# Optimization experiments

Hardware: AMD Instinct MI355X
Metric: run time of the kernel (lower is better)

Reference implementation:

```python
import jax, jax.numpy as jnp
import numpy as np

N = 100_000      # nodes
E = 3_200_000    # edges
F_IN = 9
F_HID = 9
F_OUT = 1
EPS = 1e-5

def _ln(x, g, b):
    m = x.mean(-1, keepdims=True)
    v = x.var(-1, keepdims=True)
    return (x - m) / jnp.sqrt(v + EPS) * g + b

def _gat(x, src, dst, edge_attr, W, a_src, a_dst, We, a_e, bias):
    # Single-head GATConv with edge_dim=1, add_self_loops=True, fill_value='mean'
    n = x.shape[0]
    loop = jnp.arange(n)
    deg = jax.ops.segment_sum(jnp.ones((src.shape[0],), x.dtype), dst, n)
    loop_attr = jax.ops.segment_sum(edge_attr, dst, n) / jnp.maximum(deg, 1.0)[:, None]
    s = jnp.concatenate([src, loop])
    d = jnp.concatenate([dst, loop])
    ea = jnp.concatenate([edge_attr, loop_attr], axis=0)   # [E+N, 1]
    xp = x @ W                                             # [N, C]
    a = (xp * a_src).sum(-1)[s] + (xp * a_dst).sum(-1)[d] + ((ea @ We) * a_e).sum(-1)
    a = jax.nn.leaky_relu(a, 0.2)
    amax = jax.ops.segment_max(a, d, n)
    aexp = jnp.exp(a - amax[d])
    denom = jax.ops.segment_sum(aexp, d, n)
    alpha = aexp / (denom[d] + 1e-16)
    return jax.ops.segment_sum(alpha[:, None] * xp[s], d, n) + bias

def setup_inputs() -> dict:
    key = jax.random.key(0)
    ks = jax.random.split(key, 16)
    def rn(k, shp, s):
        return jax.random.normal(k, shp, jnp.float32) * s
    return {
        "x": jax.random.normal(ks[0], (N, F_IN), jnp.float32),
        "edge_index": jax.random.randint(ks[1], (2, E), 0, N, jnp.int32),
        "edge_attr": jax.random.normal(ks[2], (E, 1), jnp.float32),
        "ln1_g": jnp.ones((F_IN,), jnp.float32), "ln1_b": jnp.zeros((F_IN,), jnp.float32),
        "W0": rn(ks[3], (F_IN, F_HID), 0.3), "as0": rn(ks[4], (F_HID,), 0.3),
        "ad0": rn(ks[5], (F_HID,), 0.3), "We0": rn(ks[6], (1, F_HID), 0.3),
        "ae0": rn(ks[7], (F_HID,), 0.3), "b0": jnp.zeros((F_HID,), jnp.float32),
        "W1": rn(ks[8], (F_HID, F_HID), 0.3), "as1": rn(ks[9], (F_HID,), 0.3),
        "ad1": rn(ks[10], (F_HID,), 0.3), "We1": rn(ks[11], (1, F_HID), 0.3),
        "ae1": rn(ks[12], (F_HID,), 0.3), "b1": jnp.zeros((F_HID,), jnp.float32),
        "ng1": jnp.ones((F_HID,), jnp.float32), "nb1": jnp.zeros((F_HID,), jnp.float32),
        "ln2_g": jnp.ones((2 * F_HID,), jnp.float32), "ln2_b": jnp.zeros((2 * F_HID,), jnp.float32),
        "et_W": rn(ks[13], (2 * F_HID, F_HID), 0.2), "et_b": jnp.zeros((F_HID,), jnp.float32),
        "fc_W": rn(ks[14], (F_HID, F_OUT), 0.3), "fc_b": jnp.zeros((F_OUT,), jnp.float32),
        "att_W": rn(ks[15], (2 * F_OUT, F_OUT), 0.5), "att_b": jnp.zeros((F_OUT,), jnp.float32),
    }

def reference(x, edge_index, edge_attr, ln1_g, ln1_b, W0, as0, ad0, We0, ae0, b0,
              W1, as1, ad1, We1, ae1, b1, ng1, nb1, ln2_g, ln2_b,
              et_W, et_b, fc_W, fc_b, att_W, att_b):
    src, dst = edge_index[0], edge_index[1]
    h = _ln(x, ln1_g, ln1_b)
    # layer 0: no norm/residual
    h = jax.nn.leaky_relu(_gat(h, src, dst, edge_attr, W0, as0, ad0, We0, ae0, b0), 0.01)
    # layer 1: norm + residual
    ident = h
    h = _ln(_gat(h, src, dst, edge_attr, W1, as1, ad1, We1, ae1, b1), ng1, nb1) + ident
    h = jax.nn.leaky_relu(h, 0.01)
    # edge path: gather-concat-norm-MLP  [E, 2H]
    ef = _ln(jnp.concatenate([h[src], h[dst]], axis=1), ln2_g, ln2_b)
    eo = jax.nn.leaky_relu(ef @ et_W + et_b, 0.01)
    eo = eo @ fc_W + fc_b                       # [E, 1]
    # AttentionLayer
    comb = jnp.concatenate([eo, edge_attr], axis=1)   # [E, 2]
    w = jax.nn.softmax(comb @ att_W + att_b, axis=-1) # [E, 1]
    att = (w * comb).sum(axis=1, keepdims=True)       # [E, 1]
    return att + eo
```

## Files before the change

kernel.cpp:

```cpp
#include <hip/hip_runtime.h>
#include <hip/hip_bf16.h>
#include <hip/hip_fp16.h>

typedef __hip_bfloat16 bf16;
typedef unsigned int uint;
typedef unsigned short ushort;
#define TPB 256
#define TPBS 1024
#define TPBG 1024
#define BSH 7
#define BNODES 128
#define NBK_MAX 1024
#define CH 8192
#define EPT (CH / TPBS)
#define NW (TPBS / 64)
#define GPAD 16
#define CAP 4608

enum {
  LN1G = 0, LN1B = 9, PW0 = 18, AS0 = 99, AD0 = 108, CE0 = 117, B0 = 118,
  PW1 = 127, AS1 = 208, AD1 = 217, CE1 = 226, B1 = 227, NG = 236, NB = 245,
  LN2G = 254, LN2B = 272, ETW = 290, ETB = 452, FCW = 461, FCB = 470,
  GC = 471, KC = 480, NPARAM = 489
};

static __device__ __forceinline__ float lrelu(float x, float s) { return x >= 0.f ? x : s * x; }
static __device__ __forceinline__ float ldx(const void* p, long i, int isb) {
    return isb ? __bfloat162float(((const bf16*)p)[i]) : ((const float*)p)[i];
}
static __device__ __forceinline__ uint bfb(float f) {
    uint u = __float_as_uint(f);
    return (u + 0x7FFFu + ((u >> 16) & 1u)) >> 16;
}
static __device__ __forceinline__ uint pack2(float a, float b) { return bfb(a) | (bfb(b) << 16); }
static __device__ __forceinline__ float unlo(uint u) { return __uint_as_float(u << 16); }
static __device__ __forceinline__ float unhi(uint u) { return __uint_as_float(u & 0xFFFF0000u); }
static __device__ __forceinline__ ushort h16(float f) { return __half_as_ushort(__float2half(f)); }
static __device__ __forceinline__ uint p2h(float a, float b) { return (uint)h16(a) | ((uint)h16(b) << 16); }
static __device__ __forceinline__ float hfl(uint u) { return __half2float(__ushort_as_half((ushort)(u & 0xFFFFu))); }
static __device__ __forceinline__ float hfh(uint u) { return __half2float(__ushort_as_half((ushort)(u >> 16))); }
static __device__ __forceinline__ float hfs(ushort u) { return __half2float(__ushort_as_half(u)); }

__global__ void k_params(const void* ln1g, const void* ln1b,
                         const void* W0, const void* as0, const void* ad0,
                         const void* We0, const void* ae0, const void* b0,
                         const void* W1, const void* as1, const void* ad1,
                         const void* We1, const void* ae1, const void* b1,
                         const void* ng, const void* nb,
                         const void* ln2g, const void* ln2b,
                         const void* etW, const void* etb,
                         const void* fcW, const void* fcb,
                         float* __restrict__ P, int* __restrict__ flagp,
                         int* __restrict__ gcursor, int nbk)
{
    __shared__ int sflag;
    if (threadIdx.x == 0) {
        unsigned short h0 = ((const unsigned short*)ln1g)[0];
        sflag = (h0 == 0x3F80u) ? 1 : 0;
        *flagp = sflag;
    }
    __syncthreads();
    const int f = sflag;
    const int t = threadIdx.x;
    for (int j = t; j < nbk; j += TPB) gcursor[j * GPAD] = j * CAP;
    for (int i = t; i < 9; i += TPB) {
        P[LN1G + i] = ldx(ln1g, i, f); P[LN1B + i] = ldx(ln1b, i, f);
        P[AS0 + i] = ldx(as0, i, f);   P[AD0 + i] = ldx(ad0, i, f);
        P[B0 + i]  = ldx(b0, i, f);
        P[AS1 + i] = ldx(as1, i, f);   P[AD1 + i] = ldx(ad1, i, f);
        P[B1 + i]  = ldx(b1, i, f);
        P[NG + i]  = ldx(ng, i, f);    P[NB + i]  = ldx(nb, i, f);
        P[ETB + i] = ldx(etb, i, f);   P[FCW + i] = ldx(fcW, i, f);
    }
    for (int i = t; i < 81; i += TPB) { P[PW0 + i] = ldx(W0, i, f); P[PW1 + i] = ldx(W1, i, f); }
    for (int i = t; i < 18; i += TPB) { P[LN2G + i] = ldx(ln2g, i, f); P[LN2B + i] = ldx(ln2b, i, f); }
    for (int i = t; i < 162; i += TPB) P[ETW + i] = ldx(etW, i, f) * ldx(ln2g, i / 9, f);
    if (t == 0) {
        float c0 = 0.f, c1 = 0.f;
        for (int k = 0; k < 9; k++) {
            c0 += ldx(We0, k, f) * ldx(ae0, k, f);
            c1 += ldx(We1, k, f) * ldx(ae1, k, f);
        }
        P[CE0] = c0; P[CE1] = c1; P[FCB] = ldx(fcb, 0, f);
        for (int c = 0; c < 9; c++) {
            float gc = 0.f, kc = 0.f;
            for (int k = 0; k < 18; k++) {
                float wv = ldx(etW, (long)k * 9 + c, f);
                gc += ldx(ln2g, k, f) * wv;
                kc += ldx(ln2b, k, f) * wv;
            }
            P[GC + c] = gc * (1.f / 18.f);
            P[KC + c] = kc + ldx(etb, c, f);
        }
    }
}

__global__ void __launch_bounds__(TPBS)
k_bscatter(const int* __restrict__ src, const int* __restrict__ dst,
           const void* __restrict__ ea, const int* __restrict__ flagp,
           int* __restrict__ gcursor, int2* __restrict__ ebuf, int e, int nbk)
{
    __shared__ int cnt[NBK_MAX];
    __shared__ int cur[NBK_MAX];
    __shared__ int badj[NBK_MAX];
    __shared__ int wsum[NW];
    __shared__ uint sidx[CH];
    const int tid = threadIdx.x;
    const int lane = tid & 63;
    const int wid = tid >> 6;
    const int s0 = blockIdx.x * CH;
    const int m = min(e - s0, CH);
    cnt[tid] = 0;
    __syncthreads();
    int dreg[EPT];
    #pragma unroll
    for (int k = 0; k < EPT; k++) {
        int t = tid + k * TPBS;
        dreg[k] = (t < m) ? dst[s0 + t] : -1;
        if (t < m) atomicAdd(&cnt[dreg[k] >> BSH], 1);
    }
    __syncthreads();
    int c = cnt[tid];
    int sc = c;
    #pragma unroll
    for (int o = 1; o < 64; o <<= 1) {
        int v = __shfl_up(sc, o, 64);
        if (lane >= o) sc += v;
    }
    if (lane == 63) wsum[wid] = sc;
    __syncthreads();
    int woff = 0;
    #pragma unroll
    for (int w = 0; w < NW; w++) woff += (w < wid) ? wsum[w] : 0;
    int ex = woff + sc - c;
    cur[tid] = ex;
    int gb = c ? atomicAdd(&gcursor[tid * GPAD], c) : 0;
    badj[tid] = gb - ex;
    __syncthreads();
    #pragma unroll
    for (int k = 0; k < EPT; k++) {
        int t = tid + k * TPBS;
        if (t < m) {
            int d = dreg[k];
            int b = d >> BSH;
            int slot = atomicAdd(&cur[b], 1);
            sidx[slot] = (uint)t | (((uint)d & (BNODES - 1)) << 13) | ((uint)b << 20);
        }
    }
    __syncthreads();
    const int fl = *flagp;
    #pragma unroll
    for (int k = 0; k < EPT; k++) {
        int j = tid + k * TPBS;
        if (j < m) {
            uint u = sidx[j];
            int t = u & 0x1FFF;
            int dl = (u >> 13) & (BNODES - 1);
            int b = u >> 20;
            int pos = badj[b] + j;
            if (pos < (b + 1) * CAP) {
                float eav = ldx(ea, s0 + t, fl);
                ebuf[pos] = make_int2(src[s0 + t] | (dl << 17), __float_as_int(eav));
            }
        }
    }
}

__global__ void k_prep(const void* __restrict__ x, const float* __restrict__ P,
                       const int* __restrict__ flagp,
                       uint* __restrict__ xpb0, float* __restrict__ sd0, int n)
{
    const int fl = *flagp;
    int i = blockIdx.x * blockDim.x + threadIdx.x;
    if (i >= n) return;
    float h[9]; float m = 0.f;
    #pragma unroll
    for (int f = 0; f < 9; f++) { h[f] = ldx(x, (long)i * 9 + f, fl); m += h[f]; }
    m *= (1.f / 9.f);
    float v = 0.f;
    #pragma unroll
    for (int f = 0; f < 9; f++) { float d = h[f] - m; v += d * d; }
    float r = rsqrtf(v * (1.f / 9.f) + 1e-5f);
    #pragma unroll
    for (int f = 0; f < 9; f++) h[f] = (h[f] - m) * r * P[LN1G + f] + P[LN1B + f];
    float xr[9]; float ss = 0.f, sd = 0.f;
    #pragma unroll
    for (int c = 0; c < 9; c++) {
        float acc = 0.f;
        #pragma unroll
        for (int f = 0; f < 9; f++) acc += h[f] * P[PW0 + f * 9 + c];
        xr[c] = acc;
        ss += acc * P[AS0 + c]; sd += acc * P[AD0 + c];
    }
    uint* row = xpb0 + (size_t)i * 8;
    ((uint4*)row)[0] = make_uint4(pack2(xr[0], xr[1]), pack2(xr[2], xr[3]),
                                  pack2(xr[4], xr[5]), pack2(xr[6], xr[7]));
    ((uint4*)row)[1] = make_uint4(pack2(xr[8], ss), 0u, 0u, 0u);
    sd0[i] = sd;
}

__global__ void __launch_bounds__(TPBG)
k_sortg0(const int* __restrict__ gcursor, const int2* __restrict__ ebuf,
         const float* __restrict__ P,
         const uint* __restrict__ xpb0, const float* __restrict__ sd0,
         float* __restrict__ h1, uint* __restrict__ xpb1,
         float* __restrict__ sd1, float* __restrict__ la, int n)
{
    __shared__ int2 seb[CAP];
    __shared__ ushort sidx[CAP];
    __shared__ int hist[BNODES], scn[BNODES], cur[BNODES];
    __shared__ int wtot[2];
    const int b = blockIdx.x, tid = threadIdx.x;
    const int beg = b * CAP;
    int cnt = gcursor[b * GPAD] - beg;
    if (cnt > CAP) cnt = CAP;
    if (cnt < 0) cnt = 0;
    if (tid < BNODES) hist[tid] = 0;
    __syncthreads();
    for (int j = tid; j < cnt; j += TPBG) {
        int2 v = ebuf[beg + j];
        seb[j] = v;
        atomicAdd(&hist[(v.x >> 17) & (BNODES - 1)], 1);
    }
    __syncthreads();
    int hc = 0, hsc = 0;
    if (tid < BNODES) {
        hc = hist[tid];
        hsc = hc;
        #pragma unroll
        for (int o = 1; o < 64; o <<= 1) {
            int v = __shfl_up(hsc, o, 64);
            if ((tid & 63) >= o) hsc += v;
        }
        if ((tid & 63) == 63) wtot[tid >> 6] = hsc;
    }
    __syncthreads();
    if (tid < BNODES) {
        int s2 = hsc + ((tid >= 64) ? wtot[0] : 0);
        scn[tid] = s2;
        cur[tid] = s2 - hc;
    }
    __syncthreads();
    for (int j = tid; j < cnt; j += TPBG) {
        int dl = (seb[j].x >> 17) & (BNODES - 1);
        int slot = atomicAdd(&cur[dl], 1);
        sidx[slot] = (ushort)j;
    }
    __syncthreads();
    const int nd = tid >> 3, l = tid & 7;
    const int i = (b << BSH) + nd;
    if (i < n) {
        const float ce = P[CE0];
        const int locend = scn[nd], locbeg = locend - hist[nd];
        const float sdi = sd0[i];
        float acc[11];
        #pragma unroll
        for (int k = 0; k < 11; k++) acc[k] = 0.f;
        for (int j = locbeg + l; j < locend; j += 8) {
            int2 sl = seb[sidx[j]];
            int s = sl.x & 0x1FFFF;
            float eav = __int_as_float(sl.y);
            const uint* row = xpb0 + (size_t)s * 8;
            uint4 q0 = *(const uint4*)row;
            uint  q2 = row[4];
            float ex = expf(lrelu(unhi(q2) + sdi + ce * eav, 0.2f));
            acc[0] += ex; acc[1] += eav;
            acc[2] += ex * unlo(q0.x); acc[3] += ex * unhi(q0.x);
            acc[4] += ex * unlo(q0.y); acc[5] += ex * unhi(q0.y);
            acc[6] += ex * unlo(q0.z); acc[7] += ex * unhi(q0.z);
            acc[8] += ex * unlo(q0.w); acc[9] += ex * unhi(q0.w);
            acc[10] += ex * unlo(q2);
        }
        #pragma unroll
        for (int k = 0; k < 11; k++) {
            acc[k] += __shfl_xor(acc[k], 1, 64);
            acc[k] += __shfl_xor(acc[k], 2, 64);
            acc[k] += __shfl_xor(acc[k], 4, 64);
        }
        if (l == 0) {
            float denom = acc[0];
            float S[9] = {acc[2], acc[3], acc[4], acc[5], acc[6], acc[7], acc[8], acc[9], acc[10]};
            float deg = (float)hist[nd];
            float lav = acc[1] / fmaxf(deg, 1.f);
            la[i] = lav;
            const uint* row = xpb0 + (size_t)i * 8;
            uint4 q0 = *(const uint4*)row;
            uint  q2 = row[4];
            float o0 = unlo(q0.x), o1 = unhi(q0.x), o2 = unlo(q0.y), o3 = unhi(q0.y);
            float o4 = unlo(q0.z), o5 = unhi(q0.z), o6 = unlo(q0.w), o7 = unhi(q0.w);
            float o8 = unlo(q2),   ssi = unhi(q2);
            float ex0 = expf(lrelu(ssi + sdi + ce * lav, 0.2f));
            denom += ex0;
            S[0] += ex0 * o0; S[1] += ex0 * o1; S[2] += ex0 * o2; S[3] += ex0 * o3;
            S[4] += ex0 * o4; S[5] += ex0 * o5; S[6] += ex0 * o6; S[7] += ex0 * o7;
            S[8] += ex0 * o8;
            float inv = 1.f / (denom + 1e-16f);
            float h[9];
            #pragma unroll
            for (int c = 0; c < 9; c++) h[c] = lrelu(S[c] * inv + P[B0 + c], 0.01f);
            float4* hr = (float4*)(h1 + (size_t)i * 12);
            hr[0] = make_float4(h[0], h[1], h[2], h[3]);
            hr[1] = make_float4(h[4], h[5], h[6], h[7]);
            hr[2] = make_float4(h[8], 0.f, 0.f, 0.f);
            float xr1[9]; float ss2 = 0.f, sd2 = 0.f;
            #pragma unroll
            for (int c = 0; c < 9; c++) {
                float a2 = 0.f;
                #pragma unroll
                for (int f = 0; f < 9; f++) a2 += h[f] * P[PW1 + f * 9 + c];
                xr1[c] = a2;
                ss2 += a2 * P[AS1 + c]; sd2 += a2 * P[AD1 + c];
            }
            uint* rw = xpb1 + (size_t)i * 8;
            ((uint4*)rw)[0] = make_uint4(pack2(xr1[0], xr1[1]), pack2(xr1[2], xr1[3]),
                                         pack2(xr1[4], xr1[5]), pack2(xr1[6], xr1[7]));
            ((uint4*)rw)[1] = make_uint4(pack2(xr1[8], ss2), 0u, 0u, 0u);
            sd1[i] = sd2;
        }
    }
}

__global__ void __launch_bounds__(TPBG)
k_sortg1(const int* __restrict__ gcursor, const int2* __restrict__ ebuf,
         const float* __restrict__ P,
         const uint* __restrict__ xpb1, const float* __restrict__ sd1,
         const float* __restrict__ la, const float* __restrict__ h1,
         uint4* __restrict__ uarr, uint4* __restrict__ warr, int n)
{
    __shared__ int2 seb[CAP];
    __shared__ ushort sidx[CAP];
    __shared__ int hist[BNODES], scn[BNODES], cur[BNODES];
    __shared__ int wtot[2];
    const int b = blockIdx.x, tid = threadIdx.x;
    const int beg = b * CAP;
    int cnt = gcursor[b * GPAD] - beg;
    if (cnt > CAP) cnt = CAP;
    if (cnt < 0) cnt = 0;
    if (tid < BNODES) hist[tid] = 0;
    __syncthreads();
    for (int j = tid; j < cnt; j += TPBG) {
        int2 v = ebuf[beg + j];
        seb[j] = v;
        atomicAdd(&hist[(v.x >> 17) & (BNODES - 1)], 1);
    }
    __syncthreads();
    int hc = 0, hsc = 0;
    if (tid < BNODES) {
        hc = hist[tid];
        hsc = hc;
        #pragma unroll
        for (int o = 1; o < 64; o <<= 1) {
            int v = __shfl_up(hsc, o, 64);
            if ((tid & 63) >= o) hsc += v;
        }
        if ((tid & 63) == 63) wtot[tid >> 6] = hsc;
    }
    __syncthreads();
    if (tid < BNODES) {
        int s2 = hsc + ((tid >= 64) ? wtot[0] : 0);
        scn[tid] = s2;
        cur[tid] = s2 - hc;
    }
    __syncthreads();
    for (int j = tid; j < cnt; j += TPBG) {
        int dl = (seb[j].x >> 17) & (BNODES - 1);
        int slot = atomicAdd(&cur[dl], 1);
        sidx[slot] = (ushort)j;
    }
    __syncthreads();
    const int nd = tid >> 3, l = tid & 7;
    const int i = (b << BSH) + nd;
    if (i < n) {
        const float ce = P[CE1];
        const int locend = scn[nd], locbeg = locend - hist[nd];
        const float sdi = sd1[i];
        float acc[10];
        #pragma unroll
        for (int k = 0; k < 10; k++) acc[k] = 0.f;
        for (int j = locbeg + l; j < locend; j += 8) {
            int2 sl = seb[sidx[j]];
            int s = sl.x & 0x1FFFF;
            float eav = __int_as_float(sl.y);
            const uint* row = xpb1 + (size_t)s * 8;
            uint4 q0 = *(const uint4*)row;
            uint  q2 = row[4];
            float ex = expf(lrelu(unhi(q2) + sdi + ce * eav, 0.2f));
            acc[0] += ex;
            acc[1] += ex * unlo(q0.x); acc[2] += ex * unhi(q0.x);
            acc[3] += ex * unlo(q0.y); acc[4] += ex * unhi(q0.y);
            acc[5] += ex * unlo(q0.z); acc[6] += ex * unhi(q0.z);
            acc[7] += ex * unlo(q0.w); acc[8] += ex * unhi(q0.w);
            acc[9] += ex * unlo(q2);
        }
        #pragma unroll
        for (int k = 0; k < 10; k++) {
            acc[k] += __shfl_xor(acc[k], 1, 64);
            acc[k] += __shfl_xor(acc[k], 2, 64);
            acc[k] += __shfl_xor(acc[k], 4, 64);
        }
        if (l == 0) {
            float denom = acc[0];
            float S[9] = {acc[1], acc[2], acc[3], acc[4], acc[5], acc[6], acc[7], acc[8], acc[9]};
            const uint* row = xpb1 + (size_t)i * 8;
            uint4 q0 = *(const uint4*)row;
            uint  q2 = row[4];
            float o0 = unlo(q0.x), o1 = unhi(q0.x), o2 = unlo(q0.y), o3 = unhi(q0.y);
            float o4 = unlo(q0.z), o5 = unhi(q0.z), o6 = unlo(q0.w), o7 = unhi(q0.w);
            float o8 = unlo(q2),   ssi = unhi(q2);
            float ex0 = expf(lrelu(ssi + sdi + ce * la[i], 0.2f));
            denom += ex0;
            S[0] += ex0 * o0; S[1] += ex0 * o1; S[2] += ex0 * o2; S[3] += ex0 * o3;
            S[4] += ex0 * o4; S[5] += ex0 * o5; S[6] += ex0 * o6; S[7] += ex0 * o7;
            S[8] += ex0 * o8;
            float inv = 1.f / (denom + 1e-16f);
            float g[9]; float m = 0.f;
            #pragma unroll
            for (int c = 0; c < 9; c++) { g[c] = S[c] * inv + P[B1 + c]; m += g[c]; }
            m *= (1.f / 9.f);
            float v = 0.f;
            #pragma unroll
            for (int c = 0; c < 9; c++) { float d = g[c] - m; v += d * d; }
            float r = rsqrtf(v * (1.f / 9.f) + 1e-5f);
            const float4* hr = (const float4*)(h1 + (size_t)i * 12);
            float4 r0 = hr[0], r1 = hr[1], r2 = hr[2];
            float res[9] = {r0.x, r0.y, r0.z, r0.w, r1.x, r1.y, r1.z, r1.w, r2.x};
            float o[9];
            #pragma unroll
            for (int c = 0; c < 9; c++)
                o[c] = lrelu((g[c] - m) * r * P[NG + c] + P[NB + c] + res[c], 0.01f);
            float psum = 0.f, pss = 0.f;
            #pragma unroll
            for (int c = 0; c < 9; c++) { psum += o[c]; pss += o[c] * o[c]; }
            uint sumb = __float_as_uint(psum * (1.f / 18.f));
            uint ssb  = __float_as_uint(pss * (1.f / 18.f));
            float u[9];
            #pragma unroll
            for (int c = 0; c < 9; c++) {
                float a2 = 0.f;
                #pragma unroll
                for (int k = 0; k < 9; k++) a2 += o[k] * P[ETW + k * 9 + c];
                u[c] = a2 - psum * P[GC + c];
            }
            uint4* up = uarr + (size_t)i * 2;
            up[0] = make_uint4(p2h(u[0], u[1]), p2h(u[2], u[3]), p2h(u[4], u[5]), p2h(u[6], u[7]));
            up[1] = make_uint4((uint)h16(u[8]), sumb, ssb, 0u);
            #pragma unroll
            for (int c = 0; c < 9; c++) {
                float a2 = 0.f;
                #pragma unroll
                for (int k = 0; k < 9; k++) a2 += o[k] * P[ETW + (9 + k) * 9 + c];
                u[c] = a2 - psum * P[GC + c];
            }
            uint4* wp = warr + (size_t)i * 2;
            wp[0] = make_uint4(p2h(u[0], u[1]), p2h(u[2], u[3]), p2h(u[4], u[5]), p2h(u[6], u[7]));
            wp[1] = make_uint4((uint)h16(u[8]), sumb, ssb, 0u);
        }
    }
}

__global__ void __launch_bounds__(TPB)
k_edge(const int* __restrict__ src, const int* __restrict__ dst,
       const void* __restrict__ ea, const float* __restrict__ P,
       const int* __restrict__ flagp,
       const uint4* __restrict__ uarr, const uint4* __restrict__ warr,
       void* __restrict__ outp, int e)
{
    const int fl = *flagp;
    int t = blockIdx.x * blockDim.x + threadIdx.x;
    if (t >= e) return;
    int s = src[t], d = dst[t];
    const uint4* up = uarr + (size_t)s * 2;
    const uint4* wp = warr + (size_t)d * 2;
    uint4 a0 = up[0], a1 = up[1];
    uint4 b0 = wp[0], b1 = wp[1];
    float m   = __uint_as_float(a1.y) + __uint_as_float(b1.y);
    float ex2 = __uint_as_float(a1.z) + __uint_as_float(b1.z);
    float r = rsqrtf(fmaxf(ex2 - m * m, 0.f) + 1e-5f);
    float uv[9] = {hfl(a0.x) + hfl(b0.x), hfh(a0.x) + hfh(b0.x),
                   hfl(a0.y) + hfl(b0.y), hfh(a0.y) + hfh(b0.y),
                   hfl(a0.z) + hfl(b0.z), hfh(a0.z) + hfh(b0.z),
                   hfl(a0.w) + hfl(b0.w), hfh(a0.w) + hfh(b0.w),
                   hfs((ushort)(a1.x & 0xFFFFu)) + hfs((ushort)(b1.x & 0xFFFFu))};
    float eo = P[FCB];
    #pragma unroll
    for (int c = 0; c < 9; c++) {
        float pre = fmaf(r, uv[c], P[KC + c]);
        float act = fmaxf(pre, 0.01f * pre);
        eo = fmaf(act, P[FCW + c], eo);
    }
    float resv = 2.f * eo + ldx(ea, t, fl);
    if (fl) ((bf16*)outp)[t] = __float2bfloat16(resv);
    else    ((float*)outp)[t] = resv;
}

extern "C" void kernel_launch(void* const* d_in, const int* in_sizes, int n_in,
                              void* d_out, int out_size, void* d_ws, size_t ws_size,
                              hipStream_t stream) {
    const int n = in_sizes[0] / 9;
    const int e = in_sizes[2];
    const int nbk = (n + BNODES - 1) >> BSH;

    const void* X   = d_in[0];
    const int*  ei  = (const int*)d_in[1];
    const int*  src = ei;
    const int*  dst = ei + e;
    const void* EA  = d_in[2];

    char* base = (char*)d_ws;
    size_t off = 0;
    auto alloc = [&](size_t bytes) { void* p = base + off; off += (bytes + 63) & ~size_t(63); return p; };
    float*  P       = (float*)alloc(512 * sizeof(float));
    int*    flagp   = (int*)(P + NPARAM);
    int*    gcursor = (int*)alloc((size_t)NBK_MAX * GPAD * sizeof(int));
    int2*   ebuf    = (int2*)alloc((size_t)nbk * CAP * sizeof(int2));
    uint*   xpb0    = (uint*)alloc((size_t)n * 8 * sizeof(uint));
    uint*   xpb1    = (uint*)alloc((size_t)n * 8 * sizeof(uint));
    float*  h1      = (float*)alloc((size_t)n * 12 * sizeof(float));
    uint4*  uarr    = (uint4*)alloc((size_t)n * 2 * sizeof(uint4));
    uint4*  warr    = (uint4*)alloc((size_t)n * 2 * sizeof(uint4));
    float*  sd0     = (float*)alloc((size_t)n * sizeof(float));
    float*  sd1     = (float*)alloc((size_t)n * sizeof(float));
    float*  la      = (float*)alloc((size_t)n * sizeof(float));

    dim3 gN((n + TPB - 1) / TPB);
    dim3 gE((e + TPB - 1) / TPB);
    dim3 gC((e + CH - 1) / CH);
    dim3 gB(nbk);

    k_params<<<1, TPB, 0, stream>>>(d_in[3], d_in[4], d_in[5], d_in[6], d_in[7],
                                    d_in[8], d_in[9], d_in[10], d_in[11], d_in[12],
                                    d_in[13], d_in[14], d_in[15], d_in[16], d_in[17],
                                    d_in[18], d_in[19], d_in[20], d_in[21], d_in[22],
                                    d_in[23], d_in[24], P, flagp, gcursor, nbk);
    k_prep<<<gN, dim3(TPB), 0, stream>>>(X, P, flagp, xpb0, sd0, n);
    k_bscatter<<<gC, dim3(TPBS), 0, stream>>>(src, dst, EA, flagp, gcursor, ebuf, e, nbk);
    k_sortg0<<<gB, dim3(TPBG), 0, stream>>>(gcursor, ebuf, P, xpb0, sd0, h1, xpb1, sd1, la, n);
    k_sortg1<<<gB, dim3(TPBG), 0, stream>>>(gcursor, ebuf, P, xpb1, sd1, la, h1, uarr, warr, n);
    k_edge<<<gE, dim3(TPB), 0, stream>>>(src, dst, EA, P, flagp, uarr, warr, d_out, e);
}
```

Before: 213.9 us.

## Store raw fp16 node features and compute edge MLP with packed dot2

Instead of precomputing two projected 9-wide vectors per node (src-role and dst-role) in k_sortg1, each node now stores only its normalized features in fp16 plus sum and sum-of-squares. The edge kernel performs the 18x9 projection itself using packed half2 dot products against fp16 weights prepared in k_params. This halves the per-node record storage and gather footprint at the cost of more arithmetic per edge. Separately, k_bscatter now loads src and edge_attr up front, keeps them in registers, and stages them through shared memory as bf16. This removes the second random global reread of src and ea, but edge_attr is rounded to bf16 in the process.

```diff
diff --git a/kernel.cpp b/kernel.cpp
--- a/kernel.cpp
+++ b/kernel.cpp
@@ -21,8 +21,19 @@
   LN1G = 0, LN1B = 9, PW0 = 18, AS0 = 99, AD0 = 108, CE0 = 117, B0 = 118,
   PW1 = 127, AS1 = 208, AD1 = 217, CE1 = 226, B1 = 227, NG = 236, NB = 245,
   LN2G = 254, LN2B = 272, ETW = 290, ETB = 452, FCW = 461, FCB = 470,
-  GC = 471, KC = 480, NPARAM = 489
+  GC = 471, KC = 480, ETH = 490, NPARAM = 580
 };
+
+#ifdef __has_builtin
+#if __has_builtin(__builtin_amdgcn_fdot2)
+#define HAVE_FDOT2 1
+#endif
+#endif
+#ifndef HAVE_FDOT2
+#define HAVE_FDOT2 0
+#endif
+
+typedef _Float16 h2f __attribute__((ext_vector_type(2)));
 
 static __device__ __forceinline__ float lrelu(float x, float s) { return x >= 0.f ? x : s * x; }
 static __device__ __forceinline__ float ldx(const void* p, long i, int isb) {
@@ -39,7 +50,14 @@
 static __device__ __forceinline__ uint p2h(float a, float b) { return (uint)h16(a) | ((uint)h16(b) << 16); }
 static __device__ __forceinline__ float hfl(uint u) { return __half2float(__ushort_as_half((ushort)(u & 0xFFFFu))); }
 static __device__ __forceinline__ float hfh(uint u) { return __half2float(__ushort_as_half((ushort)(u >> 16))); }
-static __device__ __forceinline__ float hfs(ushort u) { return __half2float(__ushort_as_half(u)); }
+static __device__ __forceinline__ h2f as_h2(uint u) { union { uint u; h2f h; } x; x.u = u; return x.h; }
+static __device__ __forceinline__ float dot2f(uint a, uint w, float acc) {
+#if HAVE_FDOT2
+    return __builtin_amdgcn_fdot2(as_h2(a), as_h2(w), acc, false);
+#else
+    return fmaf(hfl(a), hfl(w), fmaf(hfh(a), hfh(w), acc));
+#endif
+}
 
 __global__ void k_params(const void* ln1g, const void* ln1b,
                          const void* W0, const void* as0, const void* ad0,
@@ -75,6 +93,14 @@
     for (int i = t; i < 81; i += TPB) { P[PW0 + i] = ldx(W0, i, f); P[PW1 + i] = ldx(W1, i, f); }
     for (int i = t; i < 18; i += TPB) { P[LN2G + i] = ldx(ln2g, i, f); P[LN2B + i] = ldx(ln2b, i, f); }
     for (int i = t; i < 162; i += TPB) P[ETW + i] = ldx(etW, i, f) * ldx(ln2g, i / 9, f);
+    __syncthreads();
+    for (int i = t; i < 90; i += TPB) {
+        int role = i / 45, rem = i % 45, c = rem / 5, p = rem % 5;
+        int k0 = 2 * p, k1 = 2 * p + 1;
+        float w0 = (k0 < 9) ? P[ETW + (role * 9 + k0) * 9 + c] : 0.f;
+        float w1 = (k1 < 9) ? P[ETW + (role * 9 + k1) * 9 + c] : 0.f;
+        ((uint*)P)[ETH + i] = p2h(w0, w1);
+    }
     if (t == 0) {
         float c0 = 0.f, c1 = 0.f;
         for (int k = 0; k < 9; k++) {
@@ -89,7 +115,7 @@
                 gc += ldx(ln2g, k, f) * wv;
                 kc += ldx(ln2b, k, f) * wv;
             }
-            P[GC + c] = gc * (1.f / 18.f);
+            P[GC + c] = gc;
             P[KC + c] = kc + ldx(etb, c, f);
         }
     }
@@ -104,20 +130,25 @@
     __shared__ int cur[NBK_MAX];
     __shared__ int badj[NBK_MAX];
     __shared__ int wsum[NW];
-    __shared__ uint sidx[CH];
+    __shared__ int2 seb[CH];
     const int tid = threadIdx.x;
     const int lane = tid & 63;
     const int wid = tid >> 6;
     const int s0 = blockIdx.x * CH;
     const int m = min(e - s0, CH);
+    const int fl = *flagp;
     cnt[tid] = 0;
     __syncthreads();
-    int dreg[EPT];
+    int dreg[EPT]; int sreg[EPT]; float ereg[EPT];
     #pragma unroll
     for (int k = 0; k < EPT; k++) {
         int t = tid + k * TPBS;
-        dreg[k] = (t < m) ? dst[s0 + t] : -1;
-        if (t < m) atomicAdd(&cnt[dreg[k] >> BSH], 1);
+        if (t < m) {
+            dreg[k] = dst[s0 + t];
+            sreg[k] = src[s0 + t];
+            ereg[k] = ldx(ea, s0 + t, fl);
+            atomicAdd(&cnt[dreg[k] >> BSH], 1);
+        } else dreg[k] = -1;
     }
     __syncthreads();
     int c = cnt[tid];
@@ -139,28 +170,24 @@
     __syncthreads();
     #pragma unroll
     for (int k = 0; k < EPT; k++) {
-        int t = tid + k * TPBS;
-        if (t < m) {
+        if (dreg[k] >= 0) {
             int d = dreg[k];
             int b = d >> BSH;
             int slot = atomicAdd(&cur[b], 1);
-            sidx[slot] = (uint)t | (((uint)d & (BNODES - 1)) << 13) | ((uint)b << 20);
-        }
-    }
-    __syncthreads();
-    const int fl = *flagp;
+            seb[slot] = make_int2(sreg[k] | ((d & (BNODES - 1)) << 17),
+                                  (int)(bfb(ereg[k]) | ((uint)b << 16)));
+        }
+    }
+    __syncthreads();
     #pragma unroll
     for (int k = 0; k < EPT; k++) {
         int j = tid + k * TPBS;
         if (j < m) {
-            uint u = sidx[j];
-            int t = u & 0x1FFF;
-            int dl = (u >> 13) & (BNODES - 1);
-            int b = u >> 20;
+            int2 v = seb[j];
+            int b = (int)((uint)v.y >> 16);
             int pos = badj[b] + j;
             if (pos < (b + 1) * CAP) {
-                float eav = ldx(ea, s0 + t, fl);
-                ebuf[pos] = make_int2(src[s0 + t] | (dl << 17), __float_as_int(eav));
+                ebuf[pos] = make_int2(v.x, __float_as_int(unlo((uint)v.y)));
             }
         }
     }
@@ -325,7 +352,7 @@
          const float* __restrict__ P,
          const uint* __restrict__ xpb1, const float* __restrict__ sd1,
          const float* __restrict__ la, const float* __restrict__ h1,
-         uint4* __restrict__ uarr, uint4* __restrict__ warr, int n)
+         uint4* __restrict__ orec, int n)
 {
     __shared__ int2 seb[CAP];
     __shared__ ushort sidx[CAP];
@@ -431,29 +458,11 @@
             float psum = 0.f, pss = 0.f;
             #pragma unroll
             for (int c = 0; c < 9; c++) { psum += o[c]; pss += o[c] * o[c]; }
-            uint sumb = __float_as_uint(psum * (1.f / 18.f));
-            uint ssb  = __float_as_uint(pss * (1.f / 18.f));
-            float u[9];
-            #pragma unroll
-            for (int c = 0; c < 9; c++) {
-                float a2 = 0.f;
-                #pragma unroll
-                for (int k = 0; k < 9; k++) a2 += o[k] * P[ETW + k * 9 + c];
-                u[c] = a2 - psum * P[GC + c];
-            }
-            uint4* up = uarr + (size_t)i * 2;
-            up[0] = make_uint4(p2h(u[0], u[1]), p2h(u[2], u[3]), p2h(u[4], u[5]), p2h(u[6], u[7]));
-            up[1] = make_uint4((uint)h16(u[8]), sumb, ssb, 0u);
-            #pragma unroll
-            for (int c = 0; c < 9; c++) {
-                float a2 = 0.f;
-                #pragma unroll
-                for (int k = 0; k < 9; k++) a2 += o[k] * P[ETW + (9 + k) * 9 + c];
-                u[c] = a2 - psum * P[GC + c];
-            }
-            uint4* wp = warr + (size_t)i * 2;
-            wp[0] = make_uint4(p2h(u[0], u[1]), p2h(u[2], u[3]), p2h(u[4], u[5]), p2h(u[6], u[7]));
-            wp[1] = make_uint4((uint)h16(u[8]), sumb, ssb, 0u);
+            uint4* rp = orec + (size_t)i * 2;
+            rp[0] = make_uint4(p2h(o[0], o[1]), p2h(o[2], o[3]), p2h(o[4], o[5]), p2h(o[6], o[7]));
+            rp[1] = make_uint4(p2h(o[8], 0.f),
+                               __float_as_uint(psum * (1.f / 18.f)),
+                               __float_as_uint(pss * (1.f / 18.f)), 0u);
         }
     }
 }
@@ -462,29 +471,34 @@
 k_edge(const int* __restrict__ src, const int* __restrict__ dst,
        const void* __restrict__ ea, const float* __restrict__ P,
        const int* __restrict__ flagp,
-       const uint4* __restrict__ uarr, const uint4* __restrict__ warr,
-       void* __restrict__ outp, int e)
+       const uint4* __restrict__ orec, void* __restrict__ outp, int e)
 {
     const int fl = *flagp;
     int t = blockIdx.x * blockDim.x + threadIdx.x;
     if (t >= e) return;
     int s = src[t], d = dst[t];
-    const uint4* up = uarr + (size_t)s * 2;
-    const uint4* wp = warr + (size_t)d * 2;
-    uint4 a0 = up[0], a1 = up[1];
-    uint4 b0 = wp[0], b1 = wp[1];
-    float m   = __uint_as_float(a1.y) + __uint_as_float(b1.y);
-    float ex2 = __uint_as_float(a1.z) + __uint_as_float(b1.z);
+    const uint4* rs = orec + (size_t)s * 2;
+    const uint4* rd = orec + (size_t)d * 2;
+    uint4 As = rs[0], Bs = rs[1];
+    uint4 Ad = rd[0], Bd = rd[1];
+    float m   = __uint_as_float(Bs.y) + __uint_as_float(Bd.y);
+    float ex2 = __uint_as_float(Bs.z) + __uint_as_float(Bd.z);
     float r = rsqrtf(fmaxf(ex2 - m * m, 0.f) + 1e-5f);
-    float uv[9] = {hfl(a0.x) + hfl(b0.x), hfh(a0.x) + hfh(b0.x),
-                   hfl(a0.y) + hfl(b0.y), hfh(a0.y) + hfh(b0.y),
-                   hfl(a0.z) + hfl(b0.z), hfh(a0.z) + hfh(b0.z),
-                   hfl(a0.w) + hfl(b0.w), hfh(a0.w) + hfh(b0.w),
-                   hfs((ushort)(a1.x & 0xFFFFu)) + hfs((ushort)(b1.x & 0xFFFFu))};
+    const uint* eth = (const uint*)P + ETH;
     float eo = P[FCB];
     #pragma unroll
     for (int c = 0; c < 9; c++) {
-        float pre = fmaf(r, uv[c], P[KC + c]);
+        float dotc = dot2f(As.x, eth[c * 5 + 0], 0.f);
+        dotc = dot2f(As.y, eth[c * 5 + 1], dotc);
+        dotc = dot2f(As.z, eth[c * 5 + 2], dotc);
+        dotc = dot2f(As.w, eth[c * 5 + 3], dotc);
+        dotc = dot2f(Bs.x, eth[c * 5 + 4], dotc);
+        dotc = dot2f(Ad.x, eth[45 + c * 5 + 0], dotc);
+        dotc = dot2f(Ad.y, eth[45 + c * 5 + 1], dotc);
+        dotc = dot2f(Ad.z, eth[45 + c * 5 + 2], dotc);
+        dotc = dot2f(Ad.w, eth[45 + c * 5 + 3], dotc);
+        dotc = dot2f(Bd.x, eth[45 + c * 5 + 4], dotc);
+        float pre = fmaf(r, fmaf(-m, P[GC + c], dotc), P[KC + c]);
         float act = fmaxf(pre, 0.01f * pre);
         eo = fmaf(act, P[FCW + c], eo);
     }
@@ -509,15 +523,14 @@
     char* base = (char*)d_ws;
     size_t off = 0;
     auto alloc = [&](size_t bytes) { void* p = base + off; off += (bytes + 63) & ~size_t(63); return p; };
-    float*  P       = (float*)alloc(512 * sizeof(float));
+    float*  P       = (float*)alloc(1024 * sizeof(float));
     int*    flagp   = (int*)(P + NPARAM);
     int*    gcursor = (int*)alloc((size_t)NBK_MAX * GPAD * sizeof(int));
     int2*   ebuf    = (int2*)alloc((size_t)nbk * CAP * sizeof(int2));
     uint*   xpb0    = (uint*)alloc((size_t)n * 8 * sizeof(uint));
     uint*   xpb1    = (uint*)alloc((size_t)n * 8 * sizeof(uint));
     float*  h1      = (float*)alloc((size_t)n * 12 * sizeof(float));
-    uint4*  uarr    = (uint4*)alloc((size_t)n * 2 * sizeof(uint4));
-    uint4*  warr    = (uint4*)alloc((size_t)n * 2 * sizeof(uint4));
+    uint4*  orec    = (uint4*)alloc((size_t)n * 2 * sizeof(uint4));
     float*  sd0     = (float*)alloc((size_t)n * sizeof(float));
     float*  sd1     = (float*)alloc((size_t)n * sizeof(float));
     float*  la      = (float*)alloc((size_t)n * sizeof(float));
@@ -535,6 +548,6 @@
     k_prep<<<gN, dim3(TPB), 0, stream>>>(X, P, flagp, xpb0, sd0, n);
     k_bscatter<<<gC, dim3(TPBS), 0, stream>>>(src, dst, EA, flagp, gcursor, ebuf, e, nbk);
     k_sortg0<<<gB, dim3(TPBG), 0, stream>>>(gcursor, ebuf, P, xpb0, sd0, h1, xpb1, sd1, la, n);
-    k_sortg1<<<gB, dim3(TPBG), 0, stream>>>(gcursor, ebuf, P, xpb1, sd1, la, h1, uarr, warr, n);
-    k_edge<<<gE, dim3(TPB), 0, stream>>>(src, dst, EA, P, flagp, uarr, warr, d_out, e);
-}
+    k_sortg1<<<gB, dim3(TPBG), 0, stream>>>(gcursor, ebuf, P, xpb1, sd1, la, h1, orec, n);
+    k_edge<<<gE, dim3(TPB), 0, stream>>>(src, dst, EA, P, flagp, orec, d_out, e);
+}
```

After: 175.3 us. 18.0% less time.
